# Performance work log

Hardware: AMD Instinct MI355X
Metric: run time of the kernel (lower is better)

The kernel has to match this reference:

```python
import jax, jax.numpy as jnp
import numpy as np

B, C_IN, H, W = 8, 128, 64, 64
C_OUT, MID = 128, 16
EPS = 1e-5


def setup_inputs() -> dict:
    key = jax.random.key(0)
    k1, k2, k3, k4 = jax.random.split(key, 4)
    x = jax.random.normal(k1, (B, C_IN, H, W), dtype=jnp.float32)
    # per-branch 3x3 mid conv weights (bias=False): [c_out, mid, c_in, 3, 3]
    w_mid = jax.random.normal(k2, (C_OUT, MID, C_IN, 3, 3), dtype=jnp.float32) * 0.02
    # per-branch 1x1 pointwise conv (mid -> 1) weights and bias
    w_pt = jax.random.normal(k3, (C_OUT, MID), dtype=jnp.float32) * 0.1
    b_pt = jax.random.normal(k4, (C_OUT,), dtype=jnp.float32) * 0.01
    gamma = jnp.ones((C_OUT,), dtype=jnp.float32)
    beta = jnp.zeros((C_OUT,), dtype=jnp.float32)
    return {"x": x, "w_mid": w_mid, "w_pt": w_pt, "b_pt": b_pt, "gamma": gamma, "beta": beta}


def _branch_group(x, w_mid_g, w_pt_g, b_pt_g, dil):
    # w_mid_g: [R, MID, C_IN, 3, 3] -> fuse R independent full convs into one conv
    R = w_mid_g.shape[0]
    w = w_mid_g.reshape(R * MID, C_IN, 3, 3)
    y = jax.lax.conv_general_dilated(
        x, w, window_strides=(1, 1), padding=((dil, dil), (dil, dil)),
        rhs_dilation=(dil, dil), dimension_numbers=("NCHW", "OIHW", "NCHW"))
    y = y.reshape(x.shape[0], R, MID, x.shape[2], x.shape[3])
    y = jnp.where(y >= 0, y, 0.1 * y)  # LeakyReLU(0.1)
    # grouped 1x1 conv: [B,R,MID,H,W] x [R,MID] -> [B,R,H,W]
    return jnp.einsum("brmhw,rm->brhw", y, w_pt_g) + b_pt_g[None, :, None, None]


def reference(x, w_mid, w_pt, b_pt, gamma, beta):
    # even-indexed branches: pad=1, dil=1; odd-indexed: pad=2, dil=2
    ye = _branch_group(x, w_mid[0::2], w_pt[0::2], b_pt[0::2], 1)
    yo = _branch_group(x, w_mid[1::2], w_pt[1::2], b_pt[1::2], 2)
    # interleave channels back to original order: 0,1,2,...
    y = jnp.stack([ye, yo], axis=2).reshape(x.shape[0], C_OUT, x.shape[2], x.shape[3])
    # BatchNorm2d (training mode: batch stats, biased variance)
    mean = y.mean(axis=(0, 2, 3))
    var = y.var(axis=(0, 2, 3))
    yhat = (y - mean[None, :, None, None]) * jax.lax.rsqrt(var + EPS)[None, :, None, None]
    y = yhat * gamma[None, :, None, None] + beta[None, :, None, None]
    return jax.nn.relu(y)
```

## Files before the change

kernel.cpp:

```cpp
#include <hip/hip_runtime.h>
#include <hip/hip_bf16.h>

#define EPSV 1e-5f

#define WB2_ELEMS (2*4*36*256*32)
#define WB2_BYTES ((size_t)WB2_ELEMS*2)
#define XTP_ELEMS (8*68*68*128)
#define XTP_BYTES ((size_t)XTP_ELEMS*2)
#define STATS_OFF (WB2_BYTES + XTP_BYTES)

#define CONV_LDS_BYTES (131072)

typedef __attribute__((ext_vector_type(8))) short short8;
typedef __attribute__((ext_vector_type(4))) float f32x4;

__device__ __forceinline__ void gload_lds16(const void* g, void* l) {
    __builtin_amdgcn_global_load_lds(
        (const __attribute__((address_space(1))) void*)g,
        (__attribute__((address_space(3))) void*)l, 16, 0, 0);
}

__global__ __launch_bounds__(256) void k_xpad(const float* __restrict__ x,
                                              __hip_bfloat16* __restrict__ xTp) {
    int bh = blockIdx.x; int b = bh >> 6, h = bh & 63;
    __shared__ __hip_bfloat16 tile[64][130];
    int t = threadIdx.x;
#pragma unroll
    for (int i = 0; i < 32; ++i) {
        int e = (i << 8) + t; int w = e & 63; int ci = e >> 6;
        tile[w][ci] = __float2bfloat16(x[(((size_t)(b*128 + ci))*64 + h)*64 + w]);
    }
    __syncthreads();
    __hip_bfloat16* dst = xTp + ((size_t)((b*68 + h + 2)*68 + 2))*128;
#pragma unroll
    for (int i = 0; i < 32; ++i) {
        int e = (i << 8) + t; int ci = e & 127; int w = e >> 7;
        dst[w*128 + ci] = tile[w][ci];
    }
}

__global__ void k_wrepack(const float* __restrict__ w_mid,
                          __hip_bfloat16* __restrict__ wB2) {
    int idx = blockIdx.x * 256 + threadIdx.x;
    if (idx >= WB2_ELEMS) return;
    int kk  = idx & 31;
    int nl  = (idx >> 5) & 255;
    int q   = idx >> 13;
    int kt  = q % 36;
    int pnt = q / 36;
    int nt  = pnt & 3, p = pnt >> 2;
    int c_local = (nt*4 + (nl >> 6))*4 + (nl & 3);
    int m = (nl >> 2) & 15;
    int c = 2*c_local + p;
    int k = kt*32 + kk;
    int tap = k >> 7, ci = k & 127;
    wB2[idx] = __float2bfloat16(w_mid[((size_t)((c*16 + m)*128 + ci))*9 + tap]);
}

__global__ __launch_bounds__(512, 2) void k_conv(
    const __hip_bfloat16* __restrict__ xTp,
    const __hip_bfloat16* __restrict__ wB2,
    const float* __restrict__ w_pt,
    const float* __restrict__ b_pt,
    float* __restrict__ y) {
    extern __shared__ char smem[];
    __hip_bfloat16* Ae = (__hip_bfloat16*)smem;
    __hip_bfloat16* Be = (__hip_bfloat16*)(smem + 65536);

    const int combo = blockIdx.x & 7;
    const int p  = combo & 1;
    const int nt = combo >> 1;
    const int mt = blockIdx.x >> 3;
    const int dil = 1 + p;

    const int t = threadIdx.x;
    const int lane = t & 63;
    const int wave = t >> 6;
    const int wm = wave >> 2;
    const int wn = wave & 3;
    const int lm = lane & 15, lg = lane >> 4;

    const int rsub = t >> 2;
    const int ksub = (((t & 3) ^ ((t >> 3) & 3)) << 3);
    const __hip_bfloat16* abase0;
    const __hip_bfloat16* abase1;
    {
        int s0 = mt*256 + rsub;
        int s1 = s0 + 128;
        abase0 = xTp + ((size_t)(((s0>>12)*68 + ((s0>>6)&63) + 2)*68 + (s0&63) + 2))*128 + ksub;
        abase1 = xTp + ((size_t)(((s1>>12)*68 + ((s1>>6)&63) + 2)*68 + (s1&63) + 2))*128 + ksub;
    }
    const __hip_bfloat16* bbase = wB2 + (size_t)(p*4 + nt)*(36*8192)
                                + rsub*32 + ksub;

    const int sslot = (lg ^ ((lm >> 1) & 3)) << 3;
    const int aoffb = (wm*128 + lm)*32 + sslot;
    const int boffb = (wn*64 + lm)*32 + sslot;

    f32x4 acc[8][4];
#pragma unroll
    for (int i = 0; i < 8; ++i)
#pragma unroll
        for (int j = 0; j < 4; ++j) acc[i][j] = (f32x4){0.f, 0.f, 0.f, 0.f};

    {
        const int t0 = -dil*8832;
        gload_lds16(abase0 + t0,      smem           + (0*512 + t)*16);
        gload_lds16(abase1 + t0,      smem           + (1*512 + t)*16);
        gload_lds16(bbase,            smem + 65536   + (0*512 + t)*16);
        gload_lds16(bbase + 4096,     smem + 65536   + (1*512 + t)*16);
        gload_lds16(abase0 + t0 + 32, smem + 16384   + (0*512 + t)*16);
        gload_lds16(abase1 + t0 + 32, smem + 16384   + (1*512 + t)*16);
        gload_lds16(bbase + 8192,     smem + 81920   + (0*512 + t)*16);
        gload_lds16(bbase + 12288,    smem + 81920   + (1*512 + t)*16);
    }
    asm volatile("s_waitcnt vmcnt(4)" ::: "memory");
    __builtin_amdgcn_s_barrier();
    __builtin_amdgcn_sched_barrier(0);

#pragma unroll 1
    for (int vv = 0; vv < 9; ++vv) {
        const int q3c = (vv*11) >> 5;
        const int toff_c = dil*128*((q3c - 1)*68 + (vv - 3*q3c - 1));
        const int vn = vv + 1;
        const int q3n = (vn*11) >> 5;
        const int toff_n = dil*128*((q3n - 1)*68 + (vn - 3*q3n - 1));
#pragma unroll
        for (int ss = 0; ss < 4; ++ss) {
            const int d  = ss;
            const int d2 = (ss + 2) & 3;
            const bool do_stage = (vv < 8) || (ss < 2);
            short8 bf[4];
            short8 af[4];
#pragma unroll
            for (int q = 0; q < 2; ++q) {
                if (q == 0) {
#pragma unroll
                    for (int j = 0; j < 4; ++j)
                        bf[j] = *(const short8*)(Be + d*8192 + boffb + j*512);
                }
#pragma unroll
                for (int ii = 0; ii < 4; ++ii)
                    af[ii] = *(const short8*)(Ae + d*8192 + aoffb + (q*4 + ii)*512);
                if (do_stage) {
                    if (q == 0) {
                        const int aoff = (ss < 2) ? (toff_c + (ss + 2)*32)
                                                  : (toff_n + (ss - 2)*32);
                        gload_lds16(abase0 + aoff, smem + d2*16384 + (0*512 + t)*16);
                        gload_lds16(abase1 + aoff, smem + d2*16384 + (1*512 + t)*16);
                    } else {
                        const size_t bo = (size_t)(4*vv + ss + 2)*8192;
                        gload_lds16(bbase + bo,        smem + 65536 + d2*16384 + (0*512 + t)*16);
                        gload_lds16(bbase + bo + 4096, smem + 65536 + d2*16384 + (1*512 + t)*16);
                    }
                }
                if (q == 1) {
                    if (ss == 2) {
                        if (vv == 8) asm volatile("s_waitcnt vmcnt(0)" ::: "memory");
                        else         asm volatile("s_waitcnt vmcnt(4)" ::: "memory");
                    } else {
                        asm volatile("s_waitcnt vmcnt(4)" ::: "memory");
                    }
                }
                __builtin_amdgcn_s_barrier();
                asm volatile("s_waitcnt lgkmcnt(0)" ::: "memory");
                __builtin_amdgcn_sched_barrier(0);
                __builtin_amdgcn_s_setprio(1);
#pragma unroll
                for (int ii = 0; ii < 4; ++ii)
#pragma unroll
                    for (int j = 0; j < 4; ++j)
                        acc[q*4 + ii][j] = __builtin_amdgcn_mfma_f32_16x16x32_bf16(
                            af[ii], bf[j], acc[q*4 + ii][j], 0, 0, 0);
                __builtin_amdgcn_s_setprio(0);
            }
        }
    }

    {
        const int ci_ = lm & 3;
        const int mg  = lm >> 2;
        const int c   = (((nt*4 + wn)*4 + ci_) << 1) + p;
        const float bp = b_pt[c];
        float wpj[4];
#pragma unroll
        for (int j = 0; j < 4; ++j)
            wpj[j] = w_pt[c*16 + j*4 + mg];
#pragma unroll
        for (int i = 0; i < 8; ++i) {
#pragma unroll
            for (int r = 0; r < 4; ++r) {
                float s = 0.f;
#pragma unroll
                for (int j = 0; j < 4; ++j) {
                    float v = acc[i][j][r];
                    v = v >= 0.f ? v : 0.1f*v;
                    s += v * wpj[j];
                }
                s += __shfl_xor(s, 4);
                s += __shfl_xor(s, 8);
                if (mg == 0) {
                    int srow = mt*256 + wm*128 + i*16 + lg*4 + r;
                    int b = srow >> 12, hw = srow & 4095;
                    y[(size_t)(b*128 + c)*4096 + hw] = s + bp;
                }
            }
        }
    }
}

__global__ __launch_bounds__(256) void k_ystat(const float* __restrict__ y,
                                               float2* __restrict__ partials) {
    int P = blockIdx.x;
    const float4* base = (const float4*)(y + (size_t)P*4096);
    int t = threadIdx.x;
    float s = 0.f, s2 = 0.f;
#pragma unroll
    for (int i = 0; i < 4; ++i) {
        float4 v = base[t + i*256];
        s  += v.x + v.y + v.z + v.w;
        s2 += v.x*v.x + v.y*v.y + v.z*v.z + v.w*v.w;
    }
#pragma unroll
    for (int o = 32; o; o >>= 1) { s += __shfl_down(s, o); s2 += __shfl_down(s2, o); }
    __shared__ float ss[4], ss2[4];
    if ((t & 63) == 0) { ss[t >> 6] = s; ss2[t >> 6] = s2; }
    __syncthreads();
    if (t == 0)
        partials[P] = make_float2(ss[0]+ss[1]+ss[2]+ss[3], ss2[0]+ss2[1]+ss2[2]+ss2[3]);
}

__global__ __launch_bounds__(256) void k_bn_apply(float* __restrict__ y,
                                                  const float2* __restrict__ partials,
                                                  const float* __restrict__ gamma,
                                                  const float* __restrict__ beta) {
    int bid = blockIdx.x;
    int c = (bid >> 2) & 127;
    float s = 0.f, s2 = 0.f;
#pragma unroll
    for (int b = 0; b < 8; ++b) {
        float2 pr = partials[b*128 + c];
        s += pr.x; s2 += pr.y;
    }
    float mean = s * (1.f/32768.f);
    float var  = s2 * (1.f/32768.f) - mean*mean;
    float scale = gamma[c] * rsqrtf(var + EPSV);
    float shift = beta[c] - mean*scale;
    float4* y4 = (float4*)y;
    int idx = bid*256 + threadIdx.x;
    float4 v = y4[idx];
    v.x = fmaxf(v.x*scale + shift, 0.f);
    v.y = fmaxf(v.y*scale + shift, 0.f);
    v.z = fmaxf(v.z*scale + shift, 0.f);
    v.w = fmaxf(v.w*scale + shift, 0.f);
    y4[idx] = v;
}

extern "C" void kernel_launch(void* const* d_in, const int* in_sizes, int n_in,
                              void* d_out, int out_size, void* d_ws, size_t ws_size,
                              hipStream_t stream) {
    const float* x     = (const float*)d_in[0];
    const float* w_mid = (const float*)d_in[1];
    const float* w_pt  = (const float*)d_in[2];
    const float* b_pt  = (const float*)d_in[3];
    const float* gamma = (const float*)d_in[4];
    const float* beta  = (const float*)d_in[5];
    float* y = (float*)d_out;

    __hip_bfloat16* wB2 = (__hip_bfloat16*)d_ws;
    __hip_bfloat16* xTp = (__hip_bfloat16*)((char*)d_ws + WB2_BYTES);
    float2* partials    = (float2*)((char*)d_ws + STATS_OFF);

    (void)hipFuncSetAttribute((const void*)k_conv,
                              hipFuncAttributeMaxDynamicSharedMemorySize,
                              CONV_LDS_BYTES);

    hipMemsetAsync(xTp, 0, XTP_BYTES, stream);
    k_xpad<<<512, 256, 0, stream>>>(x, xTp);
    k_wrepack<<<(WB2_ELEMS + 255) / 256, 256, 0, stream>>>(w_mid, wB2);
    k_conv<<<1024, 512, CONV_LDS_BYTES, stream>>>(xTp, wB2, w_pt, b_pt, y);
    k_ystat<<<1024, 256, 0, stream>>>(y, partials);
    k_bn_apply<<<4096, 256, 0, stream>>>(y, partials, gamma, beta);
}
```

Measured before the change: 190.1 us.

## Fuse BN statistics into conv epilogue and merge prep kernels

Computes per-channel sum and sum-of-squares in the conv epilogue via shuffles and an LDS reduction, writing per-tile partials so the separate stats kernel, which re-read the whole output, is removed. The input pad/transpose and weight repack kernels are merged into one launch, and the weight repack now writes 8 bf16 values per thread. The BN apply kernel now sums 128 partials per channel instead of 8. This adds epilogue work and barriers to the conv kernel and needs a larger partials workspace.

```diff
diff --git a/kernel.cpp b/kernel.cpp
--- a/kernel.cpp
+++ b/kernel.cpp
@@ -20,41 +20,49 @@
         (__attribute__((address_space(3))) void*)l, 16, 0, 0);
 }
 
-__global__ __launch_bounds__(256) void k_xpad(const float* __restrict__ x,
-                                              __hip_bfloat16* __restrict__ xTp) {
-    int bh = blockIdx.x; int b = bh >> 6, h = bh & 63;
-    __shared__ __hip_bfloat16 tile[64][130];
+__global__ __launch_bounds__(256) void k_prep(const float* __restrict__ x,
+                                              const float* __restrict__ w_mid,
+                                              __hip_bfloat16* __restrict__ xTp,
+                                              __hip_bfloat16* __restrict__ wB2) {
     int t = threadIdx.x;
-#pragma unroll
-    for (int i = 0; i < 32; ++i) {
-        int e = (i << 8) + t; int w = e & 63; int ci = e >> 6;
-        tile[w][ci] = __float2bfloat16(x[(((size_t)(b*128 + ci))*64 + h)*64 + w]);
-    }
-    __syncthreads();
-    __hip_bfloat16* dst = xTp + ((size_t)((b*68 + h + 2)*68 + 2))*128;
-#pragma unroll
-    for (int i = 0; i < 32; ++i) {
-        int e = (i << 8) + t; int ci = e & 127; int w = e >> 7;
-        dst[w*128 + ci] = tile[w][ci];
-    }
-}
-
-__global__ void k_wrepack(const float* __restrict__ w_mid,
-                          __hip_bfloat16* __restrict__ wB2) {
-    int idx = blockIdx.x * 256 + threadIdx.x;
-    if (idx >= WB2_ELEMS) return;
-    int kk  = idx & 31;
-    int nl  = (idx >> 5) & 255;
-    int q   = idx >> 13;
-    int kt  = q % 36;
-    int pnt = q / 36;
-    int nt  = pnt & 3, p = pnt >> 2;
-    int c_local = (nt*4 + (nl >> 6))*4 + (nl & 3);
-    int m = (nl >> 2) & 15;
-    int c = 2*c_local + p;
-    int k = kt*32 + kk;
-    int tap = k >> 7, ci = k & 127;
-    wB2[idx] = __float2bfloat16(w_mid[((size_t)((c*16 + m)*128 + ci))*9 + tap]);
+    if (blockIdx.x < 512) {
+        int bh = blockIdx.x; int b = bh >> 6, h = bh & 63;
+        __shared__ __hip_bfloat16 tile[64][130];
+#pragma unroll
+        for (int i = 0; i < 32; ++i) {
+            int e = (i << 8) + t; int w = e & 63; int ci = e >> 6;
+            tile[w][ci] = __float2bfloat16(x[(((size_t)(b*128 + ci))*64 + h)*64 + w]);
+        }
+        __syncthreads();
+        __hip_bfloat16* dst = xTp + ((size_t)((b*68 + h + 2)*68 + 2))*128;
+#pragma unroll
+        for (int i = 0; i < 32; ++i) {
+            int e = (i << 8) + t; int ci = e & 127; int w = e >> 7;
+            dst[w*128 + ci] = tile[w][ci];
+        }
+    } else {
+        int e8 = (blockIdx.x - 512)*256 + t;
+        int base = e8 * 8;
+        int kk0 = base & 31;
+        int nl  = (base >> 5) & 255;
+        int q   = base >> 13;
+        int kt  = q % 36;
+        int pnt = q / 36;
+        int nt  = pnt & 3, p = pnt >> 2;
+        int c_local = (nt*4 + (nl >> 6))*4 + (nl & 3);
+        int m = (nl >> 2) & 15;
+        int c = 2*c_local + p;
+        int tap = kt >> 2;
+        int ci0 = ((kt & 3) << 5) + kk0;
+        const float* src = w_mid + ((size_t)((c*16 + m)*128 + ci0))*9 + tap;
+        short8 v;
+#pragma unroll
+        for (int e = 0; e < 8; ++e) {
+            __hip_bfloat16 h = __float2bfloat16(src[e*9]);
+            v[e] = *(short*)&h;
+        }
+        *(short8*)(wB2 + base) = v;
+    }
 }
 
 __global__ __launch_bounds__(512, 2) void k_conv(
@@ -62,7 +70,8 @@
     const __hip_bfloat16* __restrict__ wB2,
     const float* __restrict__ w_pt,
     const float* __restrict__ b_pt,
-    float* __restrict__ y) {
+    float* __restrict__ y,
+    float2* __restrict__ partials) {
     extern __shared__ char smem[];
     __hip_bfloat16* Ae = (__hip_bfloat16*)smem;
     __hip_bfloat16* Be = (__hip_bfloat16*)(smem + 65536);
@@ -186,6 +195,7 @@
 #pragma unroll
         for (int j = 0; j < 4; ++j)
             wpj[j] = w_pt[c*16 + j*4 + mg];
+        float ts = 0.f, ts2 = 0.f;
 #pragma unroll
         for (int i = 0; i < 8; ++i) {
 #pragma unroll
@@ -200,34 +210,29 @@
                 s += __shfl_xor(s, 4);
                 s += __shfl_xor(s, 8);
                 if (mg == 0) {
+                    float val = s + bp;
                     int srow = mt*256 + wm*128 + i*16 + lg*4 + r;
                     int b = srow >> 12, hw = srow & 4095;
-                    y[(size_t)(b*128 + c)*4096 + hw] = s + bp;
+                    y[(size_t)(b*128 + c)*4096 + hw] = val;
+                    ts  += val;
+                    ts2 += val*val;
                 }
             }
         }
-    }
-}
-
-__global__ __launch_bounds__(256) void k_ystat(const float* __restrict__ y,
-                                               float2* __restrict__ partials) {
-    int P = blockIdx.x;
-    const float4* base = (const float4*)(y + (size_t)P*4096);
-    int t = threadIdx.x;
-    float s = 0.f, s2 = 0.f;
-#pragma unroll
-    for (int i = 0; i < 4; ++i) {
-        float4 v = base[t + i*256];
-        s  += v.x + v.y + v.z + v.w;
-        s2 += v.x*v.x + v.y*v.y + v.z*v.z + v.w*v.w;
-    }
-#pragma unroll
-    for (int o = 32; o; o >>= 1) { s += __shfl_down(s, o); s2 += __shfl_down(s2, o); }
-    __shared__ float ss[4], ss2[4];
-    if ((t & 63) == 0) { ss[t >> 6] = s; ss2[t >> 6] = s2; }
-    __syncthreads();
-    if (t == 0)
-        partials[P] = make_float2(ss[0]+ss[1]+ss[2]+ss[3], ss2[0]+ss2[1]+ss2[2]+ss2[3]);
+        ts  += __shfl_xor(ts, 16);  ts2 += __shfl_xor(ts2, 16);
+        ts  += __shfl_xor(ts, 32);  ts2 += __shfl_xor(ts2, 32);
+        __syncthreads();
+        float2* red = (float2*)smem;
+        if (lg == 0 && mg == 0) red[wave*4 + ci_] = make_float2(ts, ts2);
+        __syncthreads();
+        if (t < 16) {
+            int wn_ = t >> 2, ci2 = t & 3;
+            float2 a0 = red[(0*4 + wn_)*4 + ci2];
+            float2 a1 = red[(1*4 + wn_)*4 + ci2];
+            int cc = (((nt*4 + wn_)*4 + ci2) << 1) + p;
+            partials[cc*128 + mt] = make_float2(a0.x + a1.x, a0.y + a1.y);
+        }
+    }
 }
 
 __global__ __launch_bounds__(256) void k_bn_apply(float* __restrict__ y,
@@ -237,9 +242,10 @@
     int bid = blockIdx.x;
     int c = (bid >> 2) & 127;
     float s = 0.f, s2 = 0.f;
-#pragma unroll
-    for (int b = 0; b < 8; ++b) {
-        float2 pr = partials[b*128 + c];
+    const float2* pc = partials + c*128;
+#pragma unroll 8
+    for (int i = 0; i < 128; ++i) {
+        float2 pr = pc[i];
         s += pr.x; s2 += pr.y;
     }
     float mean = s * (1.f/32768.f);
@@ -276,9 +282,7 @@
                               CONV_LDS_BYTES);
 
     hipMemsetAsync(xTp, 0, XTP_BYTES, stream);
-    k_xpad<<<512, 256, 0, stream>>>(x, xTp);
-    k_wrepack<<<(WB2_ELEMS + 255) / 256, 256, 0, stream>>>(w_mid, wB2);
-    k_conv<<<1024, 512, CONV_LDS_BYTES, stream>>>(xTp, wB2, w_pt, b_pt, y);
-    k_ystat<<<1024, 256, 0, stream>>>(y, partials);
+    k_prep<<<1664, 256, 0, stream>>>(x, w_mid, xTp, wB2);
+    k_conv<<<1024, 512, CONV_LDS_BYTES, stream>>>(xTp, wB2, w_pt, b_pt, y, partials);
     k_bn_apply<<<4096, 256, 0, stream>>>(y, partials, gamma, beta);
 }
```

Measured after the change: 187.6 us. About the same (-1.3%).
